# Kernel tuning notes

Measured on AMD Instinct MI355X. Metric: run time of the kernel, lower is better.

The kernel has to match this reference:

```python
import jax, jax.numpy as jnp
import numpy as np

B = 2048
C = 32            # num_categories
STATE_DIM = 64    # state_input_dim
EMB = 256         # emb_dim
OUT = 256         # output_dim
OBS_DIM = 512


def _cat_linear(x, W_all, b_all, cat_ids):
    # x: [B,S,din]; W_all: [C,din,dout]; b_all: [C,dout]; cat_ids: [B]
    W = W_all[cat_ids]            # [B,din,dout]  (per-sample weight gather)
    b = b_all[cat_ids]            # [B,dout]
    return jnp.einsum('bsd,bdh->bsh', x, W) + b[:, None, :]


def setup_inputs() -> dict:
    key = jax.random.key(0)
    ks = jax.random.split(key, 8)
    state = jax.random.normal(ks[0], (B, STATE_DIM), dtype=jnp.float32)
    obs = jax.random.uniform(ks[1], (B, 1, OBS_DIM), dtype=jnp.float32)
    cat_ids = jax.random.randint(ks[2], (B,), 0, C)
    obs_W = 0.01 * jax.random.normal(ks[3], (OBS_DIM, EMB), dtype=jnp.float32)
    obs_b = jnp.zeros((EMB,), dtype=jnp.float32)
    state_W = 0.02 * jax.random.normal(ks[4], (C, STATE_DIM, EMB), dtype=jnp.float32)
    state_b = jnp.zeros((C, EMB), dtype=jnp.float32)
    l2_W = 0.02 * jax.random.normal(ks[5], (C, 2 * EMB, OUT), dtype=jnp.float32)
    l2_b = jnp.zeros((C, OUT), dtype=jnp.float32)
    return {"state": state, "obs": obs, "cat_ids": cat_ids,
            "obs_W": obs_W, "obs_b": obs_b,
            "state_W": state_W, "state_b": state_b,
            "l2_W": l2_W, "l2_b": l2_b}


def reference(state, obs, cat_ids, obs_W, obs_b, state_W, state_b, l2_W, l2_b):
    # ObsEncoder (modeled as a linear projection): [B,1,OBS_DIM] -> [B,1,EMB]
    obs_emb = jnp.einsum('bsd,dh->bsh', obs, obs_W) + obs_b
    # state: [B,STATE_DIM] -> [B,1,STATE_DIM]
    state3 = state[:, None, :]
    state_emb = jax.nn.relu(_cat_linear(state3, state_W, state_b, cat_ids))  # [B,1,EMB]
    x = jnp.concatenate((state_emb, obs_emb), axis=2)                        # [B,1,2*EMB]
    return _cat_linear(x, l2_W, l2_b, cat_ids)                               # [B,1,OUT]
```

## Files before the change

### kernel.cpp

```cpp
#include <hip/hip_runtime.h>

constexpr int C_N   = 32;
constexpr int SD    = 64;
constexpr int OBSD  = 512;
constexpr int TILES = 16;

typedef __attribute__((ext_vector_type(8))) short bf16x8;
typedef __attribute__((ext_vector_type(4))) float f32x4;

union Frag { unsigned u[4]; bf16x8 h; };

__device__ __forceinline__ unsigned short bf_cvt(float f) {
    union { float f; unsigned u; } x; x.f = f;
    unsigned r = x.u + 0x7FFFu + ((x.u >> 16) & 1u);
    return (unsigned short)(r >> 16);
}
__device__ __forceinline__ unsigned bf_pack2(float a, float b) {
    union { float f; unsigned u; } x, y; x.f = a; y.f = b;
    unsigned ra = x.u + 0x7FFFu + ((x.u >> 16) & 1u);
    unsigned rb = y.u + 0x7FFFu + ((y.u >> 16) & 1u);
    return (ra >> 16) | (rb & 0xFFFF0000u);
}

#define LOADB(DST, WP, K0) { const float* _p = (WP) + (size_t)((K0) + quad * 8) * 256 + wcol; \
    _Pragma("unroll") for (int _j = 0; _j < 8; ++_j) { (DST)[_j] = _p[_j * 256]; (DST)[8 + _j] = _p[_j * 256 + 16]; } }

#define PACKLO(F, S) { (F).u[0] = bf_pack2((S)[0], (S)[1]);  (F).u[1] = bf_pack2((S)[2], (S)[3]); \
                       (F).u[2] = bf_pack2((S)[4], (S)[5]);  (F).u[3] = bf_pack2((S)[6], (S)[7]); }
#define PACKHI(F, S) { (F).u[0] = bf_pack2((S)[8], (S)[9]);  (F).u[1] = bf_pack2((S)[10], (S)[11]); \
                       (F).u[2] = bf_pack2((S)[12], (S)[13]); (F).u[3] = bf_pack2((S)[14], (S)[15]); }

__global__ __launch_bounds__(512, 2) void fused_kernel(
    const float* __restrict__ state, const float* __restrict__ obs,
    const int* __restrict__ cat_ids,
    const float* __restrict__ obs_W, const float* __restrict__ obs_b,
    const float* __restrict__ state_W, const float* __restrict__ state_b,
    const float* __restrict__ l2_W, const float* __restrict__ l2_b,
    float* __restrict__ out) {

    const int c = blockIdx.x;
    const int tile = blockIdx.y;
    const int t = threadIdx.x;
    const int w = t >> 6, l = t & 63;
    const int ml = l & 15, quad = l >> 4;
    const int wcol = w * 32 + ml;

    __shared__ int scnt[32];
    __shared__ int sbase[33];
    __shared__ int sRows[16];
    __shared__ __align__(16) unsigned short sAs[16 * 72];
    __shared__ __align__(16) unsigned short sAo[16 * 520];
    __shared__ __align__(16) unsigned short sX[16 * 520];

    unsigned long long mym[4];
    #pragma unroll
    for (int i = 0; i < 4; ++i) {
        int r = t + 512 * i;
        unsigned long long bal = __ballot(cat_ids[r] == c);
        mym[i] = bal;
        if (l == 0) scnt[w + 8 * i] = __popcll(bal);
    }
    __syncthreads();
    if (t == 0) {
        int run = 0;
        for (int j = 0; j < 32; ++j) { sbase[j] = run; run += scnt[j]; }
        sbase[32] = run;
    }
    __syncthreads();
    const int n = sbase[32];
    const int rbase = tile * 16;
    if (rbase >= n) return;
    const int nr = min(16, n - rbase);

    const float* pbs = state_W + (size_t)c * SD * 256;
    float r10[16], r11[16], rb0[16], rb1[16], rb2[16];
    LOADB(r10, pbs, 0)
    LOADB(r11, pbs, 32)
    LOADB(rb0, obs_W, 0)
    LOADB(rb1, obs_W, 32)
    LOADB(rb2, obs_W, 64)

    const int colb0 = wcol, colb1 = wcol + 16;
    const float bs0 = state_b[c * 256 + colb0], bs1 = state_b[c * 256 + colb1];
    const float bo0 = obs_b[colb0],             bo1 = obs_b[colb1];
    const float bl0 = l2_b[c * 256 + colb0],    bl1 = l2_b[c * 256 + colb1];

    const unsigned long long ltm = (l == 0) ? 0ull : (~0ull >> (64 - l));
    #pragma unroll
    for (int i = 0; i < 4; ++i) {
        if ((mym[i] >> l) & 1ull) {
            int s = sbase[w + 8 * i] + __popcll(mym[i] & ltm) - rbase;
            if (s >= 0 && s < 16) sRows[s] = t + 512 * i;
        }
    }
    __syncthreads();

    if (t < 256) {
        int i = t >> 4, c4 = t & 15;
        uint2 vv = make_uint2(0u, 0u);
        if (i < nr) {
            float4 v = ((const float4*)(state + (size_t)sRows[i] * SD))[c4];
            vv.x = bf_pack2(v.x, v.y); vv.y = bf_pack2(v.z, v.w);
        }
        *(uint2*)&sAs[i * 72 + c4 * 4] = vv;
    }
    #pragma unroll
    for (int i2 = 0; i2 < 4; ++i2) {
        int f = t + 512 * i2;
        int i = f >> 7, c4 = f & 127;
        uint2 vv = make_uint2(0u, 0u);
        if (i < nr) {
            float4 v = ((const float4*)(obs + (size_t)sRows[i] * OBSD))[c4];
            vv.x = bf_pack2(v.x, v.y); vv.y = bf_pack2(v.z, v.w);
        }
        *(uint2*)&sAo[i * 520 + c4 * 4] = vv;
    }
    __syncthreads();

    {
        f32x4 acc0 = {0.f, 0.f, 0.f, 0.f}, acc1 = {0.f, 0.f, 0.f, 0.f};
        bf16x8 a0 = *(const bf16x8*)&sAs[ml * 72 + quad * 8];
        bf16x8 a1 = *(const bf16x8*)&sAs[ml * 72 + 32 + quad * 8];
        Frag f0, f1;
        PACKLO(f0, r10) PACKHI(f1, r10)
        acc0 = __builtin_amdgcn_mfma_f32_16x16x32_bf16(a0, f0.h, acc0, 0, 0, 0);
        acc1 = __builtin_amdgcn_mfma_f32_16x16x32_bf16(a0, f1.h, acc1, 0, 0, 0);
        PACKLO(f0, r11) PACKHI(f1, r11)
        acc0 = __builtin_amdgcn_mfma_f32_16x16x32_bf16(a1, f0.h, acc0, 0, 0, 0);
        acc1 = __builtin_amdgcn_mfma_f32_16x16x32_bf16(a1, f1.h, acc1, 0, 0, 0);
        #pragma unroll
        for (int r = 0; r < 4; ++r) {
            sX[(quad * 4 + r) * 520 + colb0] = bf_cvt(fmaxf(acc0[r] + bs0, 0.f));
            sX[(quad * 4 + r) * 520 + colb1] = bf_cvt(fmaxf(acc1[r] + bs1, 0.f));
        }
    }

    f32x4 acc[2];
    acc[0] = (f32x4){0.f, 0.f, 0.f, 0.f};
    acc[1] = (f32x4){0.f, 0.f, 0.f, 0.f};
    {
        Frag f0, f1;
        #define P2STEP(KK, RB) { \
            bf16x8 a = *(const bf16x8*)&sAo[ml * 520 + (KK) * 32 + quad * 8]; \
            PACKLO(f0, RB) PACKHI(f1, RB) \
            if ((KK) + 3 < 16) LOADB(RB, obs_W, ((KK) + 3) * 32) \
            acc[0] = __builtin_amdgcn_mfma_f32_16x16x32_bf16(a, f0.h, acc[0], 0, 0, 0); \
            acc[1] = __builtin_amdgcn_mfma_f32_16x16x32_bf16(a, f1.h, acc[1], 0, 0, 0); }
        P2STEP(0,  rb0) P2STEP(1,  rb1) P2STEP(2,  rb2)
        P2STEP(3,  rb0) P2STEP(4,  rb1) P2STEP(5,  rb2)
        P2STEP(6,  rb0) P2STEP(7,  rb1) P2STEP(8,  rb2)
        P2STEP(9,  rb0) P2STEP(10, rb1) P2STEP(11, rb2)
        P2STEP(12, rb0) P2STEP(13, rb1) P2STEP(14, rb2)
        P2STEP(15, rb0)
        #undef P2STEP
    }

    const float* pb3 = l2_W + (size_t)c * 512 * 256;
    LOADB(rb0, pb3, 0)
    LOADB(rb1, pb3, 32)
    LOADB(rb2, pb3, 64)
    #pragma unroll
    for (int r = 0; r < 4; ++r) {
        sX[(quad * 4 + r) * 520 + 256 + colb0] = bf_cvt(acc[0][r] + bo0);
        sX[(quad * 4 + r) * 520 + 256 + colb1] = bf_cvt(acc[1][r] + bo1);
    }
    __syncthreads();

    acc[0] = (f32x4){0.f, 0.f, 0.f, 0.f};
    acc[1] = (f32x4){0.f, 0.f, 0.f, 0.f};
    {
        Frag f0, f1;
        #define P3STEP(KK, RB) { \
            bf16x8 a = *(const bf16x8*)&sX[ml * 520 + (KK) * 32 + quad * 8]; \
            PACKLO(f0, RB) PACKHI(f1, RB) \
            if ((KK) + 3 < 16) LOADB(RB, pb3, ((KK) + 3) * 32) \
            acc[0] = __builtin_amdgcn_mfma_f32_16x16x32_bf16(a, f0.h, acc[0], 0, 0, 0); \
            acc[1] = __builtin_amdgcn_mfma_f32_16x16x32_bf16(a, f1.h, acc[1], 0, 0, 0); }
        P3STEP(0,  rb0) P3STEP(1,  rb1) P3STEP(2,  rb2)
        P3STEP(3,  rb0) P3STEP(4,  rb1) P3STEP(5,  rb2)
        P3STEP(6,  rb0) P3STEP(7,  rb1) P3STEP(8,  rb2)
        P3STEP(9,  rb0) P3STEP(10, rb1) P3STEP(11, rb2)
        P3STEP(12, rb0) P3STEP(13, rb1) P3STEP(14, rb2)
        P3STEP(15, rb0)
        #undef P3STEP
    }
    #pragma unroll
    for (int r = 0; r < 4; ++r) {
        int row = quad * 4 + r;
        if (row < nr) {
            float* orow = out + (size_t)sRows[row] * 256;
            orow[colb0] = acc[0][r] + bl0;
            orow[colb1] = acc[1][r] + bl1;
        }
    }
}

extern "C" void kernel_launch(void* const* d_in, const int* in_sizes, int n_in,
                              void* d_out, int out_size, void* d_ws, size_t ws_size,
                              hipStream_t stream) {
    (void)in_sizes; (void)n_in; (void)out_size; (void)d_ws; (void)ws_size;
    fused_kernel<<<dim3(C_N, TILES), dim3(512), 0, stream>>>(
        (const float*)d_in[0],
        (const float*)d_in[1],
        (const int*)d_in[2],
        (const float*)d_in[3],
        (const float*)d_in[4],
        (const float*)d_in[5],
        (const float*)d_in[6],
        (const float*)d_in[7],
        (const float*)d_in[8],
        (float*)d_out);
}
```

Before: 98.80 us.

## Use hardware bf16 pack, deepen weight prefetch to 4 stages, parallel scan

Replaces the software round-to-nearest bf16 conversion with the v_cvt_pk_bf16_f32 instruction, and deepens the register prefetch of weight slices from 3 to 4 K-chunks in both GEMM phases. It also replaces the serial single-thread prefix sum with a wavefront shuffle scan, and hoists the bias loads to earlier in the kernel. Launch bounds drop to 1 block per SM so the extra prefetch registers fit, at the cost of lower occupancy.

Result: faster. 96.56 us (-2.3%).

```diff
diff --git a/kernel.cpp b/kernel.cpp
--- a/kernel.cpp
+++ b/kernel.cpp
@@ -10,27 +10,24 @@
 
 union Frag { unsigned u[4]; bf16x8 h; };
 
-__device__ __forceinline__ unsigned short bf_cvt(float f) {
-    union { float f; unsigned u; } x; x.f = f;
-    unsigned r = x.u + 0x7FFFu + ((x.u >> 16) & 1u);
-    return (unsigned short)(r >> 16);
-}
-__device__ __forceinline__ unsigned bf_pack2(float a, float b) {
-    union { float f; unsigned u; } x, y; x.f = a; y.f = b;
-    unsigned ra = x.u + 0x7FFFu + ((x.u >> 16) & 1u);
-    unsigned rb = y.u + 0x7FFFu + ((y.u >> 16) & 1u);
-    return (ra >> 16) | (rb & 0xFFFF0000u);
+__device__ __forceinline__ unsigned cvt_pk2(float lo, float hi) {
+    unsigned r;
+    asm("v_cvt_pk_bf16_f32 %0, %1, %2" : "=v"(r) : "v"(lo), "v"(hi));
+    return r;
+}
+__device__ __forceinline__ unsigned short cvt1(float f) {
+    return (unsigned short)cvt_pk2(f, f);
 }
 
 #define LOADB(DST, WP, K0) { const float* _p = (WP) + (size_t)((K0) + quad * 8) * 256 + wcol; \
     _Pragma("unroll") for (int _j = 0; _j < 8; ++_j) { (DST)[_j] = _p[_j * 256]; (DST)[8 + _j] = _p[_j * 256 + 16]; } }
 
-#define PACKLO(F, S) { (F).u[0] = bf_pack2((S)[0], (S)[1]);  (F).u[1] = bf_pack2((S)[2], (S)[3]); \
-                       (F).u[2] = bf_pack2((S)[4], (S)[5]);  (F).u[3] = bf_pack2((S)[6], (S)[7]); }
-#define PACKHI(F, S) { (F).u[0] = bf_pack2((S)[8], (S)[9]);  (F).u[1] = bf_pack2((S)[10], (S)[11]); \
-                       (F).u[2] = bf_pack2((S)[12], (S)[13]); (F).u[3] = bf_pack2((S)[14], (S)[15]); }
-
-__global__ __launch_bounds__(512, 2) void fused_kernel(
+#define PACKLO(F, S) { (F).u[0] = cvt_pk2((S)[0], (S)[1]);  (F).u[1] = cvt_pk2((S)[2], (S)[3]); \
+                       (F).u[2] = cvt_pk2((S)[4], (S)[5]);  (F).u[3] = cvt_pk2((S)[6], (S)[7]); }
+#define PACKHI(F, S) { (F).u[0] = cvt_pk2((S)[8], (S)[9]);  (F).u[1] = cvt_pk2((S)[10], (S)[11]); \
+                       (F).u[2] = cvt_pk2((S)[12], (S)[13]); (F).u[3] = cvt_pk2((S)[14], (S)[15]); }
+
+__global__ __launch_bounds__(512, 1) void fused_kernel(
     const float* __restrict__ state, const float* __restrict__ obs,
     const int* __restrict__ cat_ids,
     const float* __restrict__ obs_W, const float* __restrict__ obs_b,
@@ -52,6 +49,11 @@
     __shared__ __align__(16) unsigned short sAo[16 * 520];
     __shared__ __align__(16) unsigned short sX[16 * 520];
 
+    const int colb0 = wcol, colb1 = wcol + 16;
+    const float bs0 = state_b[c * 256 + colb0], bs1 = state_b[c * 256 + colb1];
+    const float bo0 = obs_b[colb0],             bo1 = obs_b[colb1];
+    const float bl0 = l2_b[c * 256 + colb0],    bl1 = l2_b[c * 256 + colb1];
+
     unsigned long long mym[4];
     #pragma unroll
     for (int i = 0; i < 4; ++i) {
@@ -61,10 +63,15 @@
         if (l == 0) scnt[w + 8 * i] = __popcll(bal);
     }
     __syncthreads();
-    if (t == 0) {
-        int run = 0;
-        for (int j = 0; j < 32; ++j) { sbase[j] = run; run += scnt[j]; }
-        sbase[32] = run;
+    if (t < 64) {
+        int v = (l < 32) ? scnt[l] : 0;
+        #pragma unroll
+        for (int d = 1; d < 32; d <<= 1) {
+            int o = __shfl_up(v, d, 64);
+            if (l >= d) v += o;
+        }
+        if (l < 32) sbase[l + 1] = v;
+        if (l == 0) sbase[0] = 0;
     }
     __syncthreads();
     const int n = sbase[32];
@@ -73,17 +80,11 @@
     const int nr = min(16, n - rbase);
 
     const float* pbs = state_W + (size_t)c * SD * 256;
-    float r10[16], r11[16], rb0[16], rb1[16], rb2[16];
+    float r10[16], r11[16], rb0[16], rb1[16], rb2[16], rb3[16];
     LOADB(r10, pbs, 0)
     LOADB(r11, pbs, 32)
     LOADB(rb0, obs_W, 0)
     LOADB(rb1, obs_W, 32)
-    LOADB(rb2, obs_W, 64)
-
-    const int colb0 = wcol, colb1 = wcol + 16;
-    const float bs0 = state_b[c * 256 + colb0], bs1 = state_b[c * 256 + colb1];
-    const float bo0 = obs_b[colb0],             bo1 = obs_b[colb1];
-    const float bl0 = l2_b[c * 256 + colb0],    bl1 = l2_b[c * 256 + colb1];
 
     const unsigned long long ltm = (l == 0) ? 0ull : (~0ull >> (64 - l));
     #pragma unroll
@@ -100,7 +101,7 @@
         uint2 vv = make_uint2(0u, 0u);
         if (i < nr) {
             float4 v = ((const float4*)(state + (size_t)sRows[i] * SD))[c4];
-            vv.x = bf_pack2(v.x, v.y); vv.y = bf_pack2(v.z, v.w);
+            vv.x = cvt_pk2(v.x, v.y); vv.y = cvt_pk2(v.z, v.w);
         }
         *(uint2*)&sAs[i * 72 + c4 * 4] = vv;
     }
@@ -111,10 +112,12 @@
         uint2 vv = make_uint2(0u, 0u);
         if (i < nr) {
             float4 v = ((const float4*)(obs + (size_t)sRows[i] * OBSD))[c4];
-            vv.x = bf_pack2(v.x, v.y); vv.y = bf_pack2(v.z, v.w);
+            vv.x = cvt_pk2(v.x, v.y); vv.y = cvt_pk2(v.z, v.w);
         }
         *(uint2*)&sAo[i * 520 + c4 * 4] = vv;
     }
+    LOADB(rb2, obs_W, 64)
+    LOADB(rb3, obs_W, 96)
     __syncthreads();
 
     {
@@ -130,8 +133,8 @@
         acc1 = __builtin_amdgcn_mfma_f32_16x16x32_bf16(a1, f1.h, acc1, 0, 0, 0);
         #pragma unroll
         for (int r = 0; r < 4; ++r) {
-            sX[(quad * 4 + r) * 520 + colb0] = bf_cvt(fmaxf(acc0[r] + bs0, 0.f));
-            sX[(quad * 4 + r) * 520 + colb1] = bf_cvt(fmaxf(acc1[r] + bs1, 0.f));
+            sX[(quad * 4 + r) * 520 + colb0] = cvt1(fmaxf(acc0[r] + bs0, 0.f));
+            sX[(quad * 4 + r) * 520 + colb1] = cvt1(fmaxf(acc1[r] + bs1, 0.f));
         }
     }
 
@@ -143,15 +146,13 @@
         #define P2STEP(KK, RB) { \
             bf16x8 a = *(const bf16x8*)&sAo[ml * 520 + (KK) * 32 + quad * 8]; \
             PACKLO(f0, RB) PACKHI(f1, RB) \
-            if ((KK) + 3 < 16) LOADB(RB, obs_W, ((KK) + 3) * 32) \
+            if ((KK) + 4 < 16) LOADB(RB, obs_W, ((KK) + 4) * 32) \
             acc[0] = __builtin_amdgcn_mfma_f32_16x16x32_bf16(a, f0.h, acc[0], 0, 0, 0); \
             acc[1] = __builtin_amdgcn_mfma_f32_16x16x32_bf16(a, f1.h, acc[1], 0, 0, 0); }
-        P2STEP(0,  rb0) P2STEP(1,  rb1) P2STEP(2,  rb2)
-        P2STEP(3,  rb0) P2STEP(4,  rb1) P2STEP(5,  rb2)
-        P2STEP(6,  rb0) P2STEP(7,  rb1) P2STEP(8,  rb2)
-        P2STEP(9,  rb0) P2STEP(10, rb1) P2STEP(11, rb2)
-        P2STEP(12, rb0) P2STEP(13, rb1) P2STEP(14, rb2)
-        P2STEP(15, rb0)
+        P2STEP(0,  rb0) P2STEP(1,  rb1) P2STEP(2,  rb2) P2STEP(3,  rb3)
+        P2STEP(4,  rb0) P2STEP(5,  rb1) P2STEP(6,  rb2) P2STEP(7,  rb3)
+        P2STEP(8,  rb0) P2STEP(9,  rb1) P2STEP(10, rb2) P2STEP(11, rb3)
+        P2STEP(12, rb0) P2STEP(13, rb1) P2STEP(14, rb2) P2STEP(15, rb3)
         #undef P2STEP
     }
 
@@ -159,10 +160,11 @@
     LOADB(rb0, pb3, 0)
     LOADB(rb1, pb3, 32)
     LOADB(rb2, pb3, 64)
+    LOADB(rb3, pb3, 96)
     #pragma unroll
     for (int r = 0; r < 4; ++r) {
-        sX[(quad * 4 + r) * 520 + 256 + colb0] = bf_cvt(acc[0][r] + bo0);
-        sX[(quad * 4 + r) * 520 + 256 + colb1] = bf_cvt(acc[1][r] + bo1);
+        sX[(quad * 4 + r) * 520 + 256 + colb0] = cvt1(acc[0][r] + bo0);
+        sX[(quad * 4 + r) * 520 + 256 + colb1] = cvt1(acc[1][r] + bo1);
     }
     __syncthreads();
 
@@ -173,15 +175,13 @@
         #define P3STEP(KK, RB) { \
             bf16x8 a = *(const bf16x8*)&sX[ml * 520 + (KK) * 32 + quad * 8]; \
             PACKLO(f0, RB) PACKHI(f1, RB) \
-            if ((KK) + 3 < 16) LOADB(RB, pb3, ((KK) + 3) * 32) \
+            if ((KK) + 4 < 16) LOADB(RB, pb3, ((KK) + 4) * 32) \
             acc[0] = __builtin_amdgcn_mfma_f32_16x16x32_bf16(a, f0.h, acc[0], 0, 0, 0); \
             acc[1] = __builtin_amdgcn_mfma_f32_16x16x32_bf16(a, f1.h, acc[1], 0, 0, 0); }
-        P3STEP(0,  rb0) P3STEP(1,  rb1) P3STEP(2,  rb2)
-        P3STEP(3,  rb0) P3STEP(4,  rb1) P3STEP(5,  rb2)
-        P3STEP(6,  rb0) P3STEP(7,  rb1) P3STEP(8,  rb2)
-        P3STEP(9,  rb0) P3STEP(10, rb1) P3STEP(11, rb2)
-        P3STEP(12, rb0) P3STEP(13, rb1) P3STEP(14, rb2)
-        P3STEP(15, rb0)
+        P3STEP(0,  rb0) P3STEP(1,  rb1) P3STEP(2,  rb2) P3STEP(3,  rb3)
+        P3STEP(4,  rb0) P3STEP(5,  rb1) P3STEP(6,  rb2) P3STEP(7,  rb3)
+        P3STEP(8,  rb0) P3STEP(9,  rb1) P3STEP(10, rb2) P3STEP(11, rb3)
+        P3STEP(12, rb0) P3STEP(13, rb1) P3STEP(14, rb2) P3STEP(15, rb3)
         #undef P3STEP
     }
     #pragma unroll
```
